# Optimization experiments

Measured on AMD Instinct MI355X. Metric: run time of the kernel, lower is better.

Reference implementation:

```python
import jax, jax.numpy as jnp
import numpy as np
from jax import lax

B, T, C_IN, HID, K, HORIZON = 64, 1024, 256, 512, 3, 12
OUT_DIM = HORIZON * 3


def causal_conv(x, w, b, dilation):
    # x: (B, C_in, T), w: (C_out, C_in, K) -> left-padded causal conv == conv+Chomp1d
    pad = (K - 1) * dilation
    y = lax.conv_general_dilated(x, w, window_strides=(1,), padding=[(pad, 0)],
                                 rhs_dilation=(dilation,),
                                 dimension_numbers=('NCH', 'OIH', 'NCH'))
    return y + b[None, :, None]


def setup_inputs() -> dict:
    key = jax.random.key(0)
    ks = jax.random.split(key, 16)
    N = B * T
    x = jax.random.normal(ks[0], (N, C_IN), jnp.float32)
    edge_index = jax.random.randint(ks[1], (2, N), 0, N, dtype=jnp.int64)
    idx = jnp.arange(N, dtype=jnp.int64)
    batch = idx // T          # graph id per node
    node_time = idx % T       # local time per node
    s1 = 1.0 / np.sqrt(C_IN * K)
    s2 = 1.0 / np.sqrt(HID * K)
    sd = 1.0 / np.sqrt(C_IN)
    sf = 1.0 / np.sqrt(HID)
    return {
        'x': x, 'edge_index': edge_index, 'batch': batch, 'node_time': node_time,
        # TemporalBlock 0 (in=C_IN, out=HID, dilation=1)
        'conv1_w0': jax.random.uniform(ks[2], (HID, C_IN, K), jnp.float32, -s1, s1),
        'conv1_b0': jax.random.uniform(ks[3], (HID,), jnp.float32, -s1, s1),
        'conv2_w0': jax.random.uniform(ks[4], (HID, HID, K), jnp.float32, -s2, s2),
        'conv2_b0': jax.random.uniform(ks[5], (HID,), jnp.float32, -s2, s2),
        'down_w0': jax.random.uniform(ks[6], (HID, C_IN, 1), jnp.float32, -sd, sd),
        'down_b0': jax.random.uniform(ks[7], (HID,), jnp.float32, -sd, sd),
        # TemporalBlock 1 (in=HID, out=HID, dilation=2, no downsample)
        'conv1_w1': jax.random.uniform(ks[8], (HID, HID, K), jnp.float32, -s2, s2),
        'conv1_b1': jax.random.uniform(ks[9], (HID,), jnp.float32, -s2, s2),
        'conv2_w1': jax.random.uniform(ks[10], (HID, HID, K), jnp.float32, -s2, s2),
        'conv2_b1': jax.random.uniform(ks[11], (HID,), jnp.float32, -s2, s2),
        # fc
        'fc_w': jax.random.uniform(ks[12], (OUT_DIM, HID), jnp.float32, -sf, sf),
        'fc_b': jax.random.uniform(ks[13], (OUT_DIM,), jnp.float32, -sf, sf),
    }


def reference(x, edge_index, batch, node_time,
              conv1_w0, conv1_b0, conv2_w0, conv2_b0, down_w0, down_b0,
              conv1_w1, conv1_b1, conv2_w1, conv2_b1, fc_w, fc_b):
    # vectorized scatter replacing the per-node Python loop
    x_seq = jnp.zeros((B, T, C_IN), x.dtype).at[batch, node_time].set(x)
    h = x_seq.transpose(0, 2, 1)  # (B, C_IN, T)
    # TemporalBlock 0 (dropout inactive in eval)
    out = jax.nn.relu(causal_conv(h, conv1_w0, conv1_b0, 1))
    out = jax.nn.relu(causal_conv(out, conv2_w0, conv2_b0, 1))
    res = jnp.einsum('bct,oc->bot', h, down_w0[:, :, 0]) + down_b0[None, :, None]
    h = jax.nn.relu(out + res)
    # TemporalBlock 1
    out = jax.nn.relu(causal_conv(h, conv1_w1, conv1_b1, 2))
    out = jax.nn.relu(causal_conv(out, conv2_w1, conv2_b1, 2))
    h = jax.nn.relu(out + h)
    # last timestep -> fc
    return h[:, :, -1] @ fc_w.T + fc_b
```

## Files before the change

kernel.cpp:

```cpp
#include <hip/hip_runtime.h>


__device__ __forceinline__ float relu(float v) { return fmaxf(v, 0.f); }

__global__ __launch_bounds__(256) void kA(const float* __restrict__ x,
                                          const float* __restrict__ w1_0,
                                          const float* __restrict__ wd0,
                                          float* __restrict__ B1a,
                                          float* __restrict__ PDa) {
  __shared__ float smem[14080];
  const int tid = threadIdx.x, lane = tid & 63, wv = tid >> 6;
  if (blockIdx.x < 256) {
    const int ocp = blockIdx.x >> 3, ks = blockIdx.x & 7, oc0 = ocp * 16;
    float* Als = smem;
    float* Bls = smem + 768;
    float acc[4][11];
#pragma unroll
    for (int i = 0; i < 4; ++i)
#pragma unroll
      for (int t = 0; t < 11; ++t) acc[i][t] = 0.f;
    for (int ch = 0; ch < 2; ++ch) {
      const int c0 = ks * 32 + ch * 16;
      if (ch) __syncthreads();
      for (int idx = tid; idx < 768; idx += 256) {
        int i = idx / 48, r = idx % 48, c = r / 3, kk = r % 3;
        Als[(c * 3 + kk) * 16 + i] = w1_0[(oc0 + i) * 768 + (c0 + c) * 3 + kk];
      }
      for (int idx = tid; idx < 13312; idx += 256) {
        int c = idx & 15, b = (idx >> 4) & 63, u = idx >> 10;
        Bls[(c * 64 + b) * 13 + u] = x[(b * 1024 + 1011 + u) * 256 + c0 + c];
      }
      __syncthreads();
      for (int c = 0; c < 16; ++c) {
        float bv[13];
#pragma unroll
        for (int u = 0; u < 13; ++u) bv[u] = Bls[(c * 64 + lane) * 13 + u];
        float av[3][4];
#pragma unroll
        for (int kk = 0; kk < 3; ++kk)
          *(float4*)av[kk] = *(const float4*)&Als[(c * 3 + kk) * 16 + wv * 4];
#pragma unroll
        for (int i = 0; i < 4; ++i)
#pragma unroll
          for (int t = 0; t < 11; ++t)
#pragma unroll
            for (int kk = 0; kk < 3; ++kk)
              acc[i][t] += av[kk][i] * bv[t + kk];
      }
    }
#pragma unroll
    for (int i = 0; i < 4; ++i)
#pragma unroll
      for (int t = 0; t < 11; ++t)
        atomicAdd(&B1a[((oc0 + wv * 4 + i) * 11 + t) * 64 + lane], acc[i][t]);
  } else {
    const int q = blockIdx.x - 256;
    const int ocp = q >> 3, ks = q & 7, oc0 = ocp * 32;
    float* Ad = smem;
    float* Bd = smem + 512;
    float acc[8][5];
#pragma unroll
    for (int i = 0; i < 8; ++i)
#pragma unroll
      for (int t = 0; t < 5; ++t) acc[i][t] = 0.f;
    for (int ch = 0; ch < 2; ++ch) {
      const int c0 = ks * 32 + ch * 16;
      if (ch) __syncthreads();
      for (int idx = tid; idx < 512; idx += 256) {
        int i = idx & 31, c = idx >> 5;
        Ad[c * 32 + i] = wd0[(oc0 + i) * 256 + c0 + c];
      }
      for (int idx = tid; idx < 5120; idx += 256) {
        int c = idx & 15, b = (idx >> 4) & 63, u = idx >> 10;
        Bd[(c * 64 + b) * 5 + u] = x[(b * 1024 + 1015 + 2 * u) * 256 + c0 + c];
      }
      __syncthreads();
      for (int c = 0; c < 16; ++c) {
        float bv[5];
#pragma unroll
        for (int u = 0; u < 5; ++u) bv[u] = Bd[(c * 64 + lane) * 5 + u];
        float av[8];
        *(float4*)&av[0] = *(const float4*)&Ad[c * 32 + wv * 8];
        *(float4*)&av[4] = *(const float4*)&Ad[c * 32 + wv * 8 + 4];
#pragma unroll
        for (int i = 0; i < 8; ++i)
#pragma unroll
          for (int t = 0; t < 5; ++t) acc[i][t] += av[i] * bv[t];
      }
    }
#pragma unroll
    for (int i = 0; i < 8; ++i)
#pragma unroll
      for (int t = 0; t < 5; ++t)
        atomicAdd(&PDa[((oc0 + wv * 8 + i) * 5 + t) * 64 + lane], acc[i][t]);
  }
}

__global__ __launch_bounds__(256) void kB(const float* __restrict__ B1a,
                                          const float* __restrict__ b1_0,
                                          const float* __restrict__ w2_0,
                                          float* __restrict__ H0a) {
  __shared__ float smem[12800];
  const int tid = threadIdx.x, lane = tid & 63, wv = tid >> 6;
  const int ocp = blockIdx.x >> 4, ks = blockIdx.x & 15, oc0 = ocp * 32;
  float* Als = smem;
  float* Bls = smem + 1536;
  float acc[8][5];
#pragma unroll
  for (int i = 0; i < 8; ++i)
#pragma unroll
    for (int t = 0; t < 5; ++t) acc[i][t] = 0.f;
  for (int ch = 0; ch < 2; ++ch) {
    const int c0 = ks * 32 + ch * 16;
    if (ch) __syncthreads();
    for (int idx = tid; idx < 1536; idx += 256) {
      int i = idx / 48, r = idx % 48, c = r / 3, kk = r % 3;
      Als[(c * 3 + kk) * 32 + i] = w2_0[(oc0 + i) * 1536 + (c0 + c) * 3 + kk];
    }
    for (int idx = tid; idx < 11264; idx += 256) {
      int b = idx & 63, u = (idx >> 6) % 11, c = (idx >> 6) / 11;
      Bls[(c * 11 + u) * 64 + b] =
          relu(B1a[((c0 + c) * 11 + u) * 64 + b] + b1_0[c0 + c]);
    }
    __syncthreads();
    for (int c = 0; c < 16; ++c) {
      float bv[11];
#pragma unroll
      for (int u = 0; u < 11; ++u) bv[u] = Bls[(c * 11 + u) * 64 + lane];
      float av[3][8];
#pragma unroll
      for (int kk = 0; kk < 3; ++kk) {
        *(float4*)&av[kk][0] = *(const float4*)&Als[(c * 3 + kk) * 32 + wv * 8];
        *(float4*)&av[kk][4] =
            *(const float4*)&Als[(c * 3 + kk) * 32 + wv * 8 + 4];
      }
#pragma unroll
      for (int i = 0; i < 8; ++i)
#pragma unroll
        for (int t = 0; t < 5; ++t)
#pragma unroll
          for (int kk = 0; kk < 3; ++kk)
            acc[i][t] += av[kk][i] * bv[2 * t + kk];
    }
  }
#pragma unroll
  for (int i = 0; i < 8; ++i)
#pragma unroll
    for (int t = 0; t < 5; ++t)
      atomicAdd(&H0a[((oc0 + wv * 8 + i) * 5 + t) * 64 + lane], acc[i][t]);
}

__global__ __launch_bounds__(256) void kC(const float* __restrict__ H0a,
                                          const float* __restrict__ b2_0,
                                          const float* __restrict__ PDa,
                                          const float* __restrict__ bd0,
                                          const float* __restrict__ w1_1,
                                          float* __restrict__ B2a) {
  __shared__ float smem[6656];
  const int tid = threadIdx.x, lane = tid & 63, wv = tid >> 6;
  const int ocp = blockIdx.x >> 4, ks = blockIdx.x & 15, oc0 = ocp * 32;
  float* Als = smem;
  float* Bls = smem + 1536;
  float acc[8][3];
#pragma unroll
  for (int i = 0; i < 8; ++i)
#pragma unroll
    for (int t = 0; t < 3; ++t) acc[i][t] = 0.f;
  for (int ch = 0; ch < 2; ++ch) {
    const int c0 = ks * 32 + ch * 16;
    if (ch) __syncthreads();
    for (int idx = tid; idx < 1536; idx += 256) {
      int i = idx / 48, r = idx % 48, c = r / 3, kk = r % 3;
      Als[(c * 3 + kk) * 32 + i] = w1_1[(oc0 + i) * 1536 + (c0 + c) * 3 + kk];
    }
    for (int idx = tid; idx < 5120; idx += 256) {
      int b = idx & 63, u = (idx >> 6) % 5, c = (idx >> 6) / 5;
      int cc = c0 + c;
      float v = relu(H0a[(cc * 5 + u) * 64 + b] + b2_0[cc]);
      Bls[(c * 5 + u) * 64 + b] = relu(v + PDa[(cc * 5 + u) * 64 + b] + bd0[cc]);
    }
    __syncthreads();
    for (int c = 0; c < 16; ++c) {
      float bv[5];
#pragma unroll
      for (int u = 0; u < 5; ++u) bv[u] = Bls[(c * 5 + u) * 64 + lane];
      float av[3][8];
#pragma unroll
      for (int kk = 0; kk < 3; ++kk) {
        *(float4*)&av[kk][0] = *(const float4*)&Als[(c * 3 + kk) * 32 + wv * 8];
        *(float4*)&av[kk][4] =
            *(const float4*)&Als[(c * 3 + kk) * 32 + wv * 8 + 4];
      }
#pragma unroll
      for (int i = 0; i < 8; ++i)
#pragma unroll
        for (int t = 0; t < 3; ++t)
#pragma unroll
          for (int kk = 0; kk < 3; ++kk)
            acc[i][t] += av[kk][i] * bv[t + kk];
    }
  }
#pragma unroll
  for (int i = 0; i < 8; ++i)
#pragma unroll
    for (int t = 0; t < 3; ++t)
      atomicAdd(&B2a[((oc0 + wv * 8 + i) * 3 + t) * 64 + lane], acc[i][t]);
}

__global__ __launch_bounds__(256) void kD(const float* __restrict__ B2a,
                                          const float* __restrict__ b1_1,
                                          const float* __restrict__ w2_1,
                                          float* __restrict__ H1a) {
  __shared__ float smem[9216];
  const int tid = threadIdx.x, lane = tid & 63, wv = tid >> 6;
  const int ocp = blockIdx.x >> 4, ks = blockIdx.x & 15, oc0 = ocp * 32;
  const int c0 = ks * 32;
  float* Als = smem;
  float* Bls = smem + 3072;
  float acc[8];
#pragma unroll
  for (int i = 0; i < 8; ++i) acc[i] = 0.f;
  for (int idx = tid; idx < 3072; idx += 256) {
    int i = idx / 96, r = idx % 96, c = r / 3, kk = r % 3;
    Als[(c * 3 + kk) * 32 + i] = w2_1[(oc0 + i) * 1536 + (c0 + c) * 3 + kk];
  }
  for (int idx = tid; idx < 6144; idx += 256) {
    int b = idx & 63, u = (idx >> 6) % 3, c = (idx >> 6) / 3;
    Bls[(c * 3 + u) * 64 + b] =
        relu(B2a[((c0 + c) * 3 + u) * 64 + b] + b1_1[c0 + c]);
  }
  __syncthreads();
  for (int c = 0; c < 32; ++c) {
    float bv[3];
#pragma unroll
    for (int u = 0; u < 3; ++u) bv[u] = Bls[(c * 3 + u) * 64 + lane];
    float av[3][8];
#pragma unroll
    for (int kk = 0; kk < 3; ++kk) {
      *(float4*)&av[kk][0] = *(const float4*)&Als[(c * 3 + kk) * 32 + wv * 8];
      *(float4*)&av[kk][4] = *(const float4*)&Als[(c * 3 + kk) * 32 + wv * 8 + 4];
    }
#pragma unroll
    for (int i = 0; i < 8; ++i)
#pragma unroll
      for (int kk = 0; kk < 3; ++kk) acc[i] += av[kk][i] * bv[kk];
  }
#pragma unroll
  for (int i = 0; i < 8; ++i)
    atomicAdd(&H1a[(oc0 + wv * 8 + i) * 64 + lane], acc[i]);
}

__global__ __launch_bounds__(256) void kE(
    const float* __restrict__ H1a, const float* __restrict__ b2_1,
    const float* __restrict__ H0a, const float* __restrict__ b2_0,
    const float* __restrict__ PDa, const float* __restrict__ bd0,
    const float* __restrict__ fcw, const float* __restrict__ fcb,
    float* __restrict__ out) {
  const int j = blockIdx.x, tid = threadIdx.x;
  const int lane = tid & 63, wv = tid >> 6;
  __shared__ float red[4][64];
  float partial = (wv == 0) ? fcb[j] : 0.f;
  for (int o = wv * 128; o < wv * 128 + 128; ++o) {
    float h0 = relu(relu(H0a[(o * 5 + 4) * 64 + lane] + b2_0[o]) +
                    PDa[(o * 5 + 4) * 64 + lane] + bd0[o]);
    float h1 = relu(relu(H1a[o * 64 + lane] + b2_1[o]) + h0);
    partial += fcw[j * 512 + o] * h1;
  }
  red[wv][lane] = partial;
  __syncthreads();
  if (wv == 0)
    out[lane * 36 + j] = red[0][lane] + red[1][lane] + red[2][lane] + red[3][lane];
}

extern "C" void kernel_launch(void* const* d_in, const int* in_sizes, int n_in,
                              void* d_out, int out_size, void* d_ws, size_t ws_size,
                              hipStream_t stream) {
  const float* x    = (const float*)d_in[0];
  const float* w1_0 = (const float*)d_in[4];
  const float* b1_0 = (const float*)d_in[5];
  const float* w2_0 = (const float*)d_in[6];
  const float* b2_0 = (const float*)d_in[7];
  const float* wd0  = (const float*)d_in[8];
  const float* bd0  = (const float*)d_in[9];
  const float* w1_1 = (const float*)d_in[10];
  const float* b1_1 = (const float*)d_in[11];
  const float* w2_1 = (const float*)d_in[12];
  const float* b2_1 = (const float*)d_in[13];
  const float* fcw  = (const float*)d_in[14];
  const float* fcb  = (const float*)d_in[15];
  float* out = (float*)d_out;

  float* B1a = (float*)d_ws;
  float* PDa = B1a + 360448;
  float* H0a = PDa + 163840;
  float* B2a = H0a + 163840;
  float* H1a = B2a + 98304;
  hipMemsetAsync(d_ws, 0, 819200 * sizeof(float), stream);

  kA<<<384, 256, 0, stream>>>(x, w1_0, wd0, B1a, PDa);
  kB<<<256, 256, 0, stream>>>(B1a, b1_0, w2_0, H0a);
  kC<<<256, 256, 0, stream>>>(H0a, b2_0, PDa, bd0, w1_1, B2a);
  kD<<<256, 256, 0, stream>>>(B2a, b1_1, w2_1, H1a);
  kE<<<36, 256, 0, stream>>>(H1a, b2_1, H0a, b2_0, PDa, bd0, fcw, fcb, out);
}
```

Before: 124.6 us.

## Replace split-K atomics with per-split partial buffers reduced in consumer kernels

Each split-K producer now writes its partial sums to a dedicated slice of a larger workspace instead of atomically adding into a zeroed buffer. The consumer kernels sum those slices with vectorized float4 loads while building their inputs. This removes the memset and the atomic contention. The x tile in shared memory gets a padded layout to avoid bank conflicts, kD is regrouped to 8 splits of 64 channels, and kC writes the final-timestep block-0 activations for kE. In exchange, workspace traffic grows because consumers read 8-16 partials per element.

```diff
diff --git a/kernel.cpp b/kernel.cpp
--- a/kernel.cpp
+++ b/kernel.cpp
@@ -2,13 +2,27 @@
 
 
 __device__ __forceinline__ float relu(float v) { return fmaxf(v, 0.f); }
+__device__ __forceinline__ float4 relu4(float4 v) {
+  v.x = fmaxf(v.x, 0.f); v.y = fmaxf(v.y, 0.f);
+  v.z = fmaxf(v.z, 0.f); v.w = fmaxf(v.w, 0.f);
+  return v;
+}
+__device__ __forceinline__ float4 add4(float4 a, float4 b) {
+  a.x += b.x; a.y += b.y; a.z += b.z; a.w += b.w;
+  return a;
+}
+__device__ __forceinline__ float4 addc4(float4 a, float c) {
+  a.x += c; a.y += c; a.z += c; a.w += c;
+  return a;
+}
+#define F4(q) (*(const float4*)(q))
 
 __global__ __launch_bounds__(256) void kA(const float* __restrict__ x,
                                           const float* __restrict__ w1_0,
                                           const float* __restrict__ wd0,
-                                          float* __restrict__ B1a,
-                                          float* __restrict__ PDa) {
-  __shared__ float smem[14080];
+                                          float* __restrict__ P0,
+                                          float* __restrict__ PD) {
+  __shared__ float smem[14288];
   const int tid = threadIdx.x, lane = tid & 63, wv = tid >> 6;
   if (blockIdx.x < 256) {
     const int ocp = blockIdx.x >> 3, ks = blockIdx.x & 7, oc0 = ocp * 16;
@@ -28,17 +42,17 @@
       }
       for (int idx = tid; idx < 13312; idx += 256) {
         int c = idx & 15, b = (idx >> 4) & 63, u = idx >> 10;
-        Bls[(c * 64 + b) * 13 + u] = x[(b * 1024 + 1011 + u) * 256 + c0 + c];
+        Bls[(c * 13 + u) * 65 + b] = x[(b * 1024 + 1011 + u) * 256 + c0 + c];
       }
       __syncthreads();
       for (int c = 0; c < 16; ++c) {
         float bv[13];
 #pragma unroll
-        for (int u = 0; u < 13; ++u) bv[u] = Bls[(c * 64 + lane) * 13 + u];
+        for (int u = 0; u < 13; ++u) bv[u] = Bls[(c * 13 + u) * 65 + lane];
         float av[3][4];
 #pragma unroll
         for (int kk = 0; kk < 3; ++kk)
-          *(float4*)av[kk] = *(const float4*)&Als[(c * 3 + kk) * 16 + wv * 4];
+          *(float4*)av[kk] = F4(&Als[(c * 3 + kk) * 16 + wv * 4]);
 #pragma unroll
         for (int i = 0; i < 4; ++i)
 #pragma unroll
@@ -52,7 +66,7 @@
     for (int i = 0; i < 4; ++i)
 #pragma unroll
       for (int t = 0; t < 11; ++t)
-        atomicAdd(&B1a[((oc0 + wv * 4 + i) * 11 + t) * 64 + lane], acc[i][t]);
+        P0[((ks * 512 + oc0 + wv * 4 + i) * 11 + t) * 64 + lane] = acc[i][t];
   } else {
     const int q = blockIdx.x - 256;
     const int ocp = q >> 3, ks = q & 7, oc0 = ocp * 32;
@@ -72,16 +86,16 @@
       }
       for (int idx = tid; idx < 5120; idx += 256) {
         int c = idx & 15, b = (idx >> 4) & 63, u = idx >> 10;
-        Bd[(c * 64 + b) * 5 + u] = x[(b * 1024 + 1015 + 2 * u) * 256 + c0 + c];
+        Bd[(c * 5 + u) * 65 + b] = x[(b * 1024 + 1015 + 2 * u) * 256 + c0 + c];
       }
       __syncthreads();
       for (int c = 0; c < 16; ++c) {
         float bv[5];
 #pragma unroll
-        for (int u = 0; u < 5; ++u) bv[u] = Bd[(c * 64 + lane) * 5 + u];
+        for (int u = 0; u < 5; ++u) bv[u] = Bd[(c * 5 + u) * 65 + lane];
         float av[8];
-        *(float4*)&av[0] = *(const float4*)&Ad[c * 32 + wv * 8];
-        *(float4*)&av[4] = *(const float4*)&Ad[c * 32 + wv * 8 + 4];
+        *(float4*)&av[0] = F4(&Ad[c * 32 + wv * 8]);
+        *(float4*)&av[4] = F4(&Ad[c * 32 + wv * 8 + 4]);
 #pragma unroll
         for (int i = 0; i < 8; ++i)
 #pragma unroll
@@ -92,14 +106,14 @@
     for (int i = 0; i < 8; ++i)
 #pragma unroll
       for (int t = 0; t < 5; ++t)
-        atomicAdd(&PDa[((oc0 + wv * 8 + i) * 5 + t) * 64 + lane], acc[i][t]);
-  }
-}
-
-__global__ __launch_bounds__(256) void kB(const float* __restrict__ B1a,
+        PD[((ks * 512 + oc0 + wv * 8 + i) * 5 + t) * 64 + lane] = acc[i][t];
+  }
+}
+
+__global__ __launch_bounds__(256) void kB(const float* __restrict__ P0,
                                           const float* __restrict__ b1_0,
                                           const float* __restrict__ w2_0,
-                                          float* __restrict__ H0a) {
+                                          float* __restrict__ P1) {
   __shared__ float smem[12800];
   const int tid = threadIdx.x, lane = tid & 63, wv = tid >> 6;
   const int ocp = blockIdx.x >> 4, ks = blockIdx.x & 15, oc0 = ocp * 32;
@@ -117,10 +131,14 @@
       int i = idx / 48, r = idx % 48, c = r / 3, kk = r % 3;
       Als[(c * 3 + kk) * 32 + i] = w2_0[(oc0 + i) * 1536 + (c0 + c) * 3 + kk];
     }
-    for (int idx = tid; idx < 11264; idx += 256) {
-      int b = idx & 63, u = (idx >> 6) % 11, c = (idx >> 6) / 11;
-      Bls[(c * 11 + u) * 64 + b] =
-          relu(B1a[((c0 + c) * 11 + u) * 64 + b] + b1_0[c0 + c]);
+    for (int idx = tid; idx < 2816; idx += 256) {
+      int c = idx / 176, r = idx % 176, u = r / 16, b4 = (r & 15) * 4;
+      int cc = c0 + c;
+      float4 s = {0.f, 0.f, 0.f, 0.f};
+#pragma unroll
+      for (int p = 0; p < 8; ++p)
+        s = add4(s, F4(&P0[((p * 512 + cc) * 11 + u) * 64 + b4]));
+      *(float4*)&Bls[(c * 11 + u) * 64 + b4] = relu4(addc4(s, b1_0[cc]));
     }
     __syncthreads();
     for (int c = 0; c < 16; ++c) {
@@ -130,9 +148,8 @@
       float av[3][8];
 #pragma unroll
       for (int kk = 0; kk < 3; ++kk) {
-        *(float4*)&av[kk][0] = *(const float4*)&Als[(c * 3 + kk) * 32 + wv * 8];
-        *(float4*)&av[kk][4] =
-            *(const float4*)&Als[(c * 3 + kk) * 32 + wv * 8 + 4];
+        *(float4*)&av[kk][0] = F4(&Als[(c * 3 + kk) * 32 + wv * 8]);
+        *(float4*)&av[kk][4] = F4(&Als[(c * 3 + kk) * 32 + wv * 8 + 4]);
       }
 #pragma unroll
       for (int i = 0; i < 8; ++i)
@@ -147,15 +164,16 @@
   for (int i = 0; i < 8; ++i)
 #pragma unroll
     for (int t = 0; t < 5; ++t)
-      atomicAdd(&H0a[((oc0 + wv * 8 + i) * 5 + t) * 64 + lane], acc[i][t]);
-}
-
-__global__ __launch_bounds__(256) void kC(const float* __restrict__ H0a,
+      P1[((ks * 512 + oc0 + wv * 8 + i) * 5 + t) * 64 + lane] = acc[i][t];
+}
+
+__global__ __launch_bounds__(256) void kC(const float* __restrict__ P1,
                                           const float* __restrict__ b2_0,
-                                          const float* __restrict__ PDa,
+                                          const float* __restrict__ PD,
                                           const float* __restrict__ bd0,
                                           const float* __restrict__ w1_1,
-                                          float* __restrict__ B2a) {
+                                          float* __restrict__ P2,
+                                          float* __restrict__ H0f) {
   __shared__ float smem[6656];
   const int tid = threadIdx.x, lane = tid & 63, wv = tid >> 6;
   const int ocp = blockIdx.x >> 4, ks = blockIdx.x & 15, oc0 = ocp * 32;
@@ -173,11 +191,21 @@
       int i = idx / 48, r = idx % 48, c = r / 3, kk = r % 3;
       Als[(c * 3 + kk) * 32 + i] = w1_1[(oc0 + i) * 1536 + (c0 + c) * 3 + kk];
     }
-    for (int idx = tid; idx < 5120; idx += 256) {
-      int b = idx & 63, u = (idx >> 6) % 5, c = (idx >> 6) / 5;
+    for (int idx = tid; idx < 1280; idx += 256) {
+      int c = idx / 80, r = idx % 80, u = r / 16, b4 = (r & 15) * 4;
       int cc = c0 + c;
-      float v = relu(H0a[(cc * 5 + u) * 64 + b] + b2_0[cc]);
-      Bls[(c * 5 + u) * 64 + b] = relu(v + PDa[(cc * 5 + u) * 64 + b] + bd0[cc]);
+      float4 s = {0.f, 0.f, 0.f, 0.f};
+#pragma unroll
+      for (int p = 0; p < 16; ++p)
+        s = add4(s, F4(&P1[((p * 512 + cc) * 5 + u) * 64 + b4]));
+      s = relu4(addc4(s, b2_0[cc]));
+      float4 d = {0.f, 0.f, 0.f, 0.f};
+#pragma unroll
+      for (int p = 0; p < 8; ++p)
+        d = add4(d, F4(&PD[((p * 512 + cc) * 5 + u) * 64 + b4]));
+      s = relu4(addc4(add4(s, d), bd0[cc]));
+      *(float4*)&Bls[(c * 5 + u) * 64 + b4] = s;
+      if (ocp == 0 && u == 4) *(float4*)&H0f[cc * 64 + b4] = s;
     }
     __syncthreads();
     for (int c = 0; c < 16; ++c) {
@@ -187,9 +215,8 @@
       float av[3][8];
 #pragma unroll
       for (int kk = 0; kk < 3; ++kk) {
-        *(float4*)&av[kk][0] = *(const float4*)&Als[(c * 3 + kk) * 32 + wv * 8];
-        *(float4*)&av[kk][4] =
-            *(const float4*)&Als[(c * 3 + kk) * 32 + wv * 8 + 4];
+        *(float4*)&av[kk][0] = F4(&Als[(c * 3 + kk) * 32 + wv * 8]);
+        *(float4*)&av[kk][4] = F4(&Als[(c * 3 + kk) * 32 + wv * 8 + 4]);
       }
 #pragma unroll
       for (int i = 0; i < 8; ++i)
@@ -204,41 +231,45 @@
   for (int i = 0; i < 8; ++i)
 #pragma unroll
     for (int t = 0; t < 3; ++t)
-      atomicAdd(&B2a[((oc0 + wv * 8 + i) * 3 + t) * 64 + lane], acc[i][t]);
-}
-
-__global__ __launch_bounds__(256) void kD(const float* __restrict__ B2a,
+      P2[((ks * 512 + oc0 + wv * 8 + i) * 3 + t) * 64 + lane] = acc[i][t];
+}
+
+__global__ __launch_bounds__(256) void kD(const float* __restrict__ P2,
                                           const float* __restrict__ b1_1,
                                           const float* __restrict__ w2_1,
-                                          float* __restrict__ H1a) {
-  __shared__ float smem[9216];
+                                          float* __restrict__ P3) {
+  __shared__ float smem[18432];
   const int tid = threadIdx.x, lane = tid & 63, wv = tid >> 6;
-  const int ocp = blockIdx.x >> 4, ks = blockIdx.x & 15, oc0 = ocp * 32;
-  const int c0 = ks * 32;
+  const int ocp = blockIdx.x >> 3, ks = blockIdx.x & 7, oc0 = ocp * 32;
+  const int c0 = ks * 64;
   float* Als = smem;
-  float* Bls = smem + 3072;
+  float* Bls = smem + 6144;
   float acc[8];
 #pragma unroll
   for (int i = 0; i < 8; ++i) acc[i] = 0.f;
+  for (int idx = tid; idx < 6144; idx += 256) {
+    int i = idx / 192, r = idx % 192, c = r / 3, kk = r % 3;
+    Als[(c * 3 + kk) * 32 + i] = w2_1[(oc0 + i) * 1536 + (c0 + c) * 3 + kk];
+  }
   for (int idx = tid; idx < 3072; idx += 256) {
-    int i = idx / 96, r = idx % 96, c = r / 3, kk = r % 3;
-    Als[(c * 3 + kk) * 32 + i] = w2_1[(oc0 + i) * 1536 + (c0 + c) * 3 + kk];
-  }
-  for (int idx = tid; idx < 6144; idx += 256) {
-    int b = idx & 63, u = (idx >> 6) % 3, c = (idx >> 6) / 3;
-    Bls[(c * 3 + u) * 64 + b] =
-        relu(B2a[((c0 + c) * 3 + u) * 64 + b] + b1_1[c0 + c]);
+    int c = idx / 48, r = idx % 48, u = r / 16, b4 = (r & 15) * 4;
+    int cc = c0 + c;
+    float4 s = {0.f, 0.f, 0.f, 0.f};
+#pragma unroll
+    for (int p = 0; p < 16; ++p)
+      s = add4(s, F4(&P2[((p * 512 + cc) * 3 + u) * 64 + b4]));
+    *(float4*)&Bls[(c * 3 + u) * 64 + b4] = relu4(addc4(s, b1_1[cc]));
   }
   __syncthreads();
-  for (int c = 0; c < 32; ++c) {
+  for (int c = 0; c < 64; ++c) {
     float bv[3];
 #pragma unroll
     for (int u = 0; u < 3; ++u) bv[u] = Bls[(c * 3 + u) * 64 + lane];
     float av[3][8];
 #pragma unroll
     for (int kk = 0; kk < 3; ++kk) {
-      *(float4*)&av[kk][0] = *(const float4*)&Als[(c * 3 + kk) * 32 + wv * 8];
-      *(float4*)&av[kk][4] = *(const float4*)&Als[(c * 3 + kk) * 32 + wv * 8 + 4];
+      *(float4*)&av[kk][0] = F4(&Als[(c * 3 + kk) * 32 + wv * 8]);
+      *(float4*)&av[kk][4] = F4(&Als[(c * 3 + kk) * 32 + wv * 8 + 4]);
     }
 #pragma unroll
     for (int i = 0; i < 8; ++i)
@@ -247,29 +278,31 @@
   }
 #pragma unroll
   for (int i = 0; i < 8; ++i)
-    atomicAdd(&H1a[(oc0 + wv * 8 + i) * 64 + lane], acc[i]);
-}
-
-__global__ __launch_bounds__(256) void kE(
-    const float* __restrict__ H1a, const float* __restrict__ b2_1,
-    const float* __restrict__ H0a, const float* __restrict__ b2_0,
-    const float* __restrict__ PDa, const float* __restrict__ bd0,
-    const float* __restrict__ fcw, const float* __restrict__ fcb,
-    float* __restrict__ out) {
+    P3[(ks * 512 + oc0 + wv * 8 + i) * 64 + lane] = acc[i];
+}
+
+__global__ __launch_bounds__(256) void kE(const float* __restrict__ P3,
+                                          const float* __restrict__ b2_1,
+                                          const float* __restrict__ H0f,
+                                          const float* __restrict__ fcw,
+                                          const float* __restrict__ fcb,
+                                          float* __restrict__ out) {
   const int j = blockIdx.x, tid = threadIdx.x;
   const int lane = tid & 63, wv = tid >> 6;
   __shared__ float red[4][64];
   float partial = (wv == 0) ? fcb[j] : 0.f;
   for (int o = wv * 128; o < wv * 128 + 128; ++o) {
-    float h0 = relu(relu(H0a[(o * 5 + 4) * 64 + lane] + b2_0[o]) +
-                    PDa[(o * 5 + 4) * 64 + lane] + bd0[o]);
-    float h1 = relu(relu(H1a[o * 64 + lane] + b2_1[o]) + h0);
+    float s = 0.f;
+#pragma unroll
+    for (int p = 0; p < 8; ++p) s += P3[(p * 512 + o) * 64 + lane];
+    float h1 = relu(relu(s + b2_1[o]) + H0f[o * 64 + lane]);
     partial += fcw[j * 512 + o] * h1;
   }
   red[wv][lane] = partial;
   __syncthreads();
   if (wv == 0)
-    out[lane * 36 + j] = red[0][lane] + red[1][lane] + red[2][lane] + red[3][lane];
+    out[lane * 36 + j] =
+        red[0][lane] + red[1][lane] + red[2][lane] + red[3][lane];
 }
 
 extern "C" void kernel_launch(void* const* d_in, const int* in_sizes, int n_in,
@@ -290,16 +323,16 @@
   const float* fcb  = (const float*)d_in[15];
   float* out = (float*)d_out;
 
-  float* B1a = (float*)d_ws;
-  float* PDa = B1a + 360448;
-  float* H0a = PDa + 163840;
-  float* B2a = H0a + 163840;
-  float* H1a = B2a + 98304;
-  hipMemsetAsync(d_ws, 0, 819200 * sizeof(float), stream);
-
-  kA<<<384, 256, 0, stream>>>(x, w1_0, wd0, B1a, PDa);
-  kB<<<256, 256, 0, stream>>>(B1a, b1_0, w2_0, H0a);
-  kC<<<256, 256, 0, stream>>>(H0a, b2_0, PDa, bd0, w1_1, B2a);
-  kD<<<256, 256, 0, stream>>>(B2a, b1_1, w2_1, H1a);
-  kE<<<36, 256, 0, stream>>>(H1a, b2_1, H0a, b2_0, PDa, bd0, fcw, fcb, out);
-}
+  float* P0  = (float*)d_ws;
+  float* PD  = P0 + 2883584;
+  float* P1  = PD + 1310720;
+  float* P2  = P1 + 2621440;
+  float* P3  = P2 + 1572864;
+  float* H0f = P3 + 262144;
+
+  kA<<<384, 256, 0, stream>>>(x, w1_0, wd0, P0, PD);
+  kB<<<256, 256, 0, stream>>>(P0, b1_0, w2_0, P1);
+  kC<<<256, 256, 0, stream>>>(P1, b2_0, PD, bd0, w1_1, P2, H0f);
+  kD<<<128, 256, 0, stream>>>(P2, b1_1, w2_1, P3);
+  kE<<<36, 256, 0, stream>>>(P3, b2_1, H0f, fcw, fcb, out);
+}
```

New measurement: 125.4 us. No clear change (+0.6%).
